# Kernel tuning notes

Measured on AMD Instinct MI355X. Metric: run time of the kernel, lower is better.

Reference implementation:

```python
import jax, jax.numpy as jnp
import numpy as np

FP8_MAX = 448.0   # float8_e4m3fn max magnitude
BS = 128          # quantization block size


def setup_inputs() -> dict:
    key = jax.random.key(0)
    k1, k2 = jax.random.split(key)
    M, K, N = 4096, 4096, 16384
    x = jax.random.normal(k1, (M, K), jnp.float32)
    # Build an FP8 block-quantized weight the way load() expects it:
    # weight holds fp8-representable values, weight_scale_inv is per 128x128 block.
    w = jax.random.normal(k2, (N, K), jnp.float32) * 0.02
    wb = w.reshape(N // BS, BS, K // BS, BS)
    amax = jnp.max(jnp.abs(wb), axis=(1, 3))            # [N/BS, K/BS]
    weight_scale_inv = amax / FP8_MAX                    # fp32 block scales
    wq = (wb / weight_scale_inv[:, None, :, None]).astype(jnp.float8_e4m3fn)
    weight = wq.astype(jnp.float32).reshape(N, K)        # fp8 values held in fp32
    return {"x": x, "weight": weight, "weight_scale_inv": weight_scale_inv}


def reference(x, weight, weight_scale_inv):
    M, K = x.shape
    N = weight.shape[0]
    # --- act_quant: per-(row, 128-block) FP8 quantization of activations ---
    xb = x.reshape(M, K // BS, BS)
    s_x = jnp.max(jnp.abs(xb), axis=-1) / FP8_MAX        # [M, K/BS] fp32 scales
    xq = (xb / s_x[..., None]).astype(jnp.float8_e4m3fn) # simulate fp8 rounding
    # --- fp8_gemm: scaled GEMM with inline dequantization ---
    x_dq = (xq.astype(jnp.float32) * s_x[..., None]).reshape(M, K)
    w_dq = (weight.reshape(N // BS, BS, K // BS, BS)
            * weight_scale_inv[:, None, :, None]).reshape(N, K)
    # y[m, n] = sum_k x_dq[m, k] * w_dq[n, k]
    return jnp.einsum('mk,nk->mn', x_dq, w_dq)
```

## Files before the change

### kernel.cpp

```cpp
#include <hip/hip_runtime.h>
#include <stdint.h>

#define FP8_MAX 448.0f
#define BSQ 128
#define TM 128
#define TN 128
#define NKB 32

typedef int   i32x4  __attribute__((ext_vector_type(4)));
typedef int   i32x8  __attribute__((ext_vector_type(8)));
typedef float f32x4v __attribute__((ext_vector_type(4)));
typedef float f32x16 __attribute__((ext_vector_type(16)));

typedef const __attribute__((address_space(1))) uint8_t* gptr_t;
typedef __attribute__((address_space(3))) uint8_t* lptr_t;

__device__ __forceinline__ int hsw(int row) { return (row ^ (row >> 3)) & 7; }

__global__ void act_quant_kernel(const float* __restrict__ x,
                                 uint8_t* __restrict__ xq,
                                 float* __restrict__ sxT,
                                 int M, int K) {
    int gid  = blockIdx.x * blockDim.x + threadIdx.x;
    int wave = gid >> 6;
    int lane = threadIdx.x & 63;
    int nkb  = K / BSQ;
    int row  = wave / nkb;
    int kb   = wave - row * nkb;
    if (row >= M) return;

    const float2 v = *(const float2*)(x + (size_t)row * K + kb * BSQ + lane * 2);
    float am = fmaxf(fabsf(v.x), fabsf(v.y));
#pragma unroll
    for (int off = 32; off >= 1; off >>= 1)
        am = fmaxf(am, __shfl_xor(am, off));

    float s = am / FP8_MAX;
    if (lane == 0) sxT[(size_t)kb * M + row] = s;

    float q0 = (am > 0.f) ? v.x / s : 0.f;
    float q1 = (am > 0.f) ? v.y / s : 0.f;
    int packed = __builtin_amdgcn_cvt_pk_fp8_f32(q0, q1, 0, false);
    *(uint16_t*)(xq + (size_t)row * K + kb * BSQ + lane * 2) = (uint16_t)(packed & 0xffff);
}

__global__ void weight_quant_kernel(const float* __restrict__ w,
                                    uint8_t* __restrict__ wq, size_t n) {
    size_t i = ((size_t)blockIdx.x * blockDim.x + threadIdx.x) * 4;
    if (i >= n) return;
    float4 v = *(const float4*)(w + i);
    int lo = __builtin_amdgcn_cvt_pk_fp8_f32(v.x, v.y, 0, false);
    int hi = __builtin_amdgcn_cvt_pk_fp8_f32(v.z, v.w, 0, false);
    *(uint32_t*)(wq + i) = (uint32_t)((lo & 0xffff) | (hi << 16));
}

__global__ __launch_bounds__(256, 2)
void fp8_gemm_mx(const uint8_t* __restrict__ Aq,
                 const uint8_t* __restrict__ Bq,
                 const float*  __restrict__ sxT,
                 const float*  __restrict__ swg,
                 float* __restrict__ out,
                 int M, int N, int K) {
    __shared__ uint8_t As[2][TM * BSQ];
    __shared__ uint8_t Bs[2][TN * BSQ];
    __shared__ float   sxs[2][TM];

    const int tid  = threadIdx.x;
    const int lane = tid & 63;
    const int wid  = tid >> 6;
    const int brow = blockIdx.y * TM;
    const int bcol = blockIdx.x * TN;
    const int nb   = bcol >> 7;

    const int wy = wid >> 1, wx = wid & 1;
    const int fl = lane & 31, hi = lane >> 5;

    auto STAGE = [&](int buf, int kb) {
#pragma unroll
        for (int r = 0; r < 4; ++r) {
            int slot = r * 256 + tid;
            int row  = slot >> 3;
            int g    = (slot & 7) ^ hsw(row);
            const uint8_t* gA = Aq + (size_t)(brow + row) * K + kb * BSQ + g * 16;
            const uint8_t* gB = Bq + (size_t)(bcol + row) * K + kb * BSQ + g * 16;
            __builtin_amdgcn_global_load_lds((gptr_t)gA,
                (lptr_t)(As[buf] + (slot & ~63) * 16), 16, 0, 0);
            __builtin_amdgcn_global_load_lds((gptr_t)gB,
                (lptr_t)(Bs[buf] + (slot & ~63) * 16), 16, 0, 0);
        }
        if (wid < 2) {
            const float* gs = sxT + (size_t)kb * M + brow + wid * 64 + lane;
            __builtin_amdgcn_global_load_lds((gptr_t)(const uint8_t*)gs,
                (lptr_t)(sxs[buf] + wid * 64), 4, 0, 0);
        }
    };

    const f32x16 zz = {0.f,0.f,0.f,0.f, 0.f,0.f,0.f,0.f,
                       0.f,0.f,0.f,0.f, 0.f,0.f,0.f,0.f};
    f32x16 acc[2][2];
#pragma unroll
    for (int i = 0; i < 2; ++i)
#pragma unroll
        for (int j = 0; j < 2; ++j) acc[i][j] = zz;

    STAGE(0, 0);
    __syncthreads();

    for (int kb = 0; kb < NKB; ++kb) {
        const int cur = kb & 1;
        const uint8_t* Ab = As[cur];
        const uint8_t* Bb = Bs[cur];
        const float*   Sb = sxs[cur];

        if (kb + 1 < NKB) STAGE(cur ^ 1, kb + 1);

        const float sw = swg[(size_t)nb * NKB + kb];

        i32x8 bfr[2][2];
#pragma unroll
        for (int fn = 0; fn < 2; ++fn) {
            int row = wx * 64 + fn * 32 + fl;
            int hh  = hsw(row);
            const uint8_t* base = Bb + row * BSQ;
#pragma unroll
            for (int kh = 0; kh < 2; ++kh) {
                int g0 = kh * 4 + hi * 2;
                i32x4 lo = *(const i32x4*)(base + (((g0    ) ^ hh) << 4));
                i32x4 h4 = *(const i32x4*)(base + (((g0 + 1) ^ hh) << 4));
                bfr[fn][kh] = (i32x8){lo.x, lo.y, lo.z, lo.w, h4.x, h4.y, h4.z, h4.w};
            }
        }

#pragma unroll
        for (int fm = 0; fm < 2; ++fm) {
            int arow = wy * 64 + fm * 32 + fl;
            int hh   = hsw(arow);
            const uint8_t* abase = Ab + arow * BSQ;
            i32x8 afr[2];
#pragma unroll
            for (int kh = 0; kh < 2; ++kh) {
                int g0 = kh * 4 + hi * 2;
                i32x4 lo = *(const i32x4*)(abase + (((g0    ) ^ hh) << 4));
                i32x4 h4 = *(const i32x4*)(abase + (((g0 + 1) ^ hh) << 4));
                afr[kh] = (i32x8){lo.x, lo.y, lo.z, lo.w, h4.x, h4.y, h4.z, h4.w};
            }
            f32x4v s4[4];
#pragma unroll
            for (int q = 0; q < 4; ++q) {
                s4[q] = *(const f32x4v*)&Sb[wy * 64 + fm * 32 + q * 8 + hi * 4];
                s4[q] *= sw;
            }

#pragma unroll
            for (int fn = 0; fn < 2; ++fn) {
                f32x16 p = __builtin_amdgcn_mfma_scale_f32_32x32x64_f8f6f4(
                    afr[0], bfr[fn][0], zz, 0, 0, 0, 127, 0, 127);
                p = __builtin_amdgcn_mfma_scale_f32_32x32x64_f8f6f4(
                    afr[1], bfr[fn][1], p, 0, 0, 0, 127, 0, 127);
#pragma unroll
                for (int q = 0; q < 4; ++q)
#pragma unroll
                    for (int j = 0; j < 4; ++j)
                        acc[fm][fn][q * 4 + j] += p[q * 4 + j] * s4[q][j];
            }
        }

        __syncthreads();
    }

#pragma unroll
    for (int fm = 0; fm < 2; ++fm)
#pragma unroll
        for (int fn = 0; fn < 2; ++fn)
#pragma unroll
            for (int q = 0; q < 4; ++q)
#pragma unroll
                for (int j = 0; j < 4; ++j) {
                    int row = brow + wy * 64 + fm * 32 + q * 8 + hi * 4 + j;
                    int col = bcol + wx * 64 + fn * 32 + fl;
                    __builtin_nontemporal_store(acc[fm][fn][q * 4 + j],
                                                &out[(size_t)row * N + col]);
                }
}

extern "C" void kernel_launch(void* const* d_in, const int* in_sizes, int n_in,
                              void* d_out, int out_size, void* d_ws, size_t ws_size,
                              hipStream_t stream) {
    const float* x   = (const float*)d_in[0];
    const float* w   = (const float*)d_in[1];
    const float* wsi = (const float*)d_in[2];
    float* out = (float*)d_out;

    const int K = 4096;
    const int M = in_sizes[0] / K;
    const int N = in_sizes[1] / K;

    uint8_t* xq  = (uint8_t*)d_ws;
    uint8_t* wq  = xq + (size_t)M * K;
    float*   sxT = (float*)(wq + (size_t)N * K);

    int waves = M * (K / BSQ);
    act_quant_kernel<<<dim3(waves / 4), dim3(256), 0, stream>>>(x, xq, sxT, M, K);

    size_t wn = (size_t)N * K;
    weight_quant_kernel<<<dim3((unsigned)(wn / 4 / 256)), dim3(256), 0, stream>>>(w, wq, wn);

    dim3 grid(N / TN, M / TM);
    fp8_gemm_mx<<<grid, dim3(256), 0, stream>>>(xq, wq, sxT, wsi, out, M, N, K);
}
```

Measured before the change: 458.4 us.

## Split K-block staging into two phases with fine-grained vmcnt waits and barriers

Replaces the single STAGE-plus-__syncthreads double buffering with a split prefetch. The B tile, scales and the first half of the A rows are issued after the B fragments are read, and the second half of the A rows after the first A fragment group is consumed. Explicit s_waitcnt vmcnt counts and raw s_barrier calls let each fm half start once only its own data has landed. It also interleaves the two MFMA chains and raises wave priority around them. The hand-counted vmcnt values depend on the exact number of global_load_lds instructions issued per lane, so a miscount could race or stall.

After: 478.1 us. 1.04x slower.

```diff
diff --git a/kernel.cpp b/kernel.cpp
--- a/kernel.cpp
+++ b/kernel.cpp
@@ -75,23 +75,48 @@
     const int wy = wid >> 1, wx = wid & 1;
     const int fl = lane & 31, hi = lane >> 5;
 
-    auto STAGE = [&](int buf, int kb) {
-#pragma unroll
-        for (int r = 0; r < 4; ++r) {
+    auto ISSUE7 = [&](int buf, int kb) {
+        {
+            if (lane < 32) {
+                const float* gs = sxT + (size_t)kb * M + brow + wid * 32 + lane;
+                __builtin_amdgcn_global_load_lds((gptr_t)(const uint8_t*)gs,
+                    (lptr_t)(sxs[buf] + wid * 32), 4, 0, 0);
+            }
+        }
+#pragma unroll
+        for (int h = 0; h < 2; ++h)
+#pragma unroll
+            for (int r = 0; r < 2; ++r) {
+                int slot = r * 256 + tid;
+                int row  = h * 64 + (slot >> 3);
+                int g    = (slot & 7) ^ hsw(row);
+                const uint8_t* gB = Bq + (size_t)(bcol + row) * K + kb * BSQ + g * 16;
+                __builtin_amdgcn_global_load_lds((gptr_t)gB,
+                    (lptr_t)(Bs[buf] + h * 8192 + (slot & ~63) * 16), 16, 0, 0);
+            }
+#pragma unroll
+        for (int r = 0; r < 2; ++r) {
             int slot = r * 256 + tid;
-            int row  = slot >> 3;
+            int rp   = slot >> 3;
+            int row  = (rp & 31) + ((rp & 32) << 1);
             int g    = (slot & 7) ^ hsw(row);
             const uint8_t* gA = Aq + (size_t)(brow + row) * K + kb * BSQ + g * 16;
-            const uint8_t* gB = Bq + (size_t)(bcol + row) * K + kb * BSQ + g * 16;
+            int rp0  = (r * 256 + wid * 64) >> 3;
             __builtin_amdgcn_global_load_lds((gptr_t)gA,
-                (lptr_t)(As[buf] + (slot & ~63) * 16), 16, 0, 0);
-            __builtin_amdgcn_global_load_lds((gptr_t)gB,
-                (lptr_t)(Bs[buf] + (slot & ~63) * 16), 16, 0, 0);
-        }
-        if (wid < 2) {
-            const float* gs = sxT + (size_t)kb * M + brow + wid * 64 + lane;
-            __builtin_amdgcn_global_load_lds((gptr_t)(const uint8_t*)gs,
-                (lptr_t)(sxs[buf] + wid * 64), 4, 0, 0);
+                (lptr_t)(As[buf] + ((rp0 & 31) + ((rp0 & 32) << 1)) * 128), 16, 0, 0);
+        }
+    };
+    auto ISSUE2 = [&](int buf, int kb) {
+#pragma unroll
+        for (int r = 0; r < 2; ++r) {
+            int slot = r * 256 + tid;
+            int rp   = slot >> 3;
+            int row  = 32 + (rp & 31) + ((rp & 32) << 1);
+            int g    = (slot & 7) ^ hsw(row);
+            const uint8_t* gA = Aq + (size_t)(brow + row) * K + kb * BSQ + g * 16;
+            int rp0  = (r * 256 + wid * 64) >> 3;
+            __builtin_amdgcn_global_load_lds((gptr_t)gA,
+                (lptr_t)(As[buf] + (32 + (rp0 & 31) + ((rp0 & 32) << 1)) * 128), 16, 0, 0);
         }
     };
 
@@ -103,18 +128,20 @@
 #pragma unroll
         for (int j = 0; j < 2; ++j) acc[i][j] = zz;
 
-    STAGE(0, 0);
-    __syncthreads();
+    ISSUE7(0, 0);
+    ISSUE2(0, 0);
 
     for (int kb = 0; kb < NKB; ++kb) {
         const int cur = kb & 1;
+        const bool pf = (kb + 1 < NKB);
         const uint8_t* Ab = As[cur];
         const uint8_t* Bb = Bs[cur];
         const float*   Sb = sxs[cur];
-
-        if (kb + 1 < NKB) STAGE(cur ^ 1, kb + 1);
-
         const float sw = swg[(size_t)nb * NKB + kb];
+
+        asm volatile("s_waitcnt vmcnt(2)" ::: "memory");
+        __builtin_amdgcn_s_barrier();
+        asm volatile("" ::: "memory");
 
         i32x8 bfr[2][2];
 #pragma unroll
@@ -131,8 +158,17 @@
             }
         }
 
+        if (pf) ISSUE7(cur ^ 1, kb + 1);
+
 #pragma unroll
         for (int fm = 0; fm < 2; ++fm) {
+            if (fm == 1) {
+                if (pf) asm volatile("s_waitcnt vmcnt(7)" ::: "memory");
+                else    asm volatile("s_waitcnt vmcnt(0)" ::: "memory");
+                __builtin_amdgcn_s_barrier();
+                asm volatile("" ::: "memory");
+            }
+
             int arow = wy * 64 + fm * 32 + fl;
             int hh   = hsw(arow);
             const uint8_t* abase = Ab + arow * BSQ;
@@ -151,21 +187,27 @@
                 s4[q] *= sw;
             }
 
-#pragma unroll
-            for (int fn = 0; fn < 2; ++fn) {
-                f32x16 p = __builtin_amdgcn_mfma_scale_f32_32x32x64_f8f6f4(
-                    afr[0], bfr[fn][0], zz, 0, 0, 0, 127, 0, 127);
-                p = __builtin_amdgcn_mfma_scale_f32_32x32x64_f8f6f4(
-                    afr[1], bfr[fn][1], p, 0, 0, 0, 127, 0, 127);
-#pragma unroll
-                for (int q = 0; q < 4; ++q)
-#pragma unroll
-                    for (int j = 0; j < 4; ++j)
-                        acc[fm][fn][q * 4 + j] += p[q * 4 + j] * s4[q][j];
-            }
-        }
-
-        __syncthreads();
+            if (fm == 1 && pf) ISSUE2(cur ^ 1, kb + 1);
+
+            __builtin_amdgcn_s_setprio(1);
+            f32x16 p0 = __builtin_amdgcn_mfma_scale_f32_32x32x64_f8f6f4(
+                afr[0], bfr[0][0], zz, 0, 0, 0, 127, 0, 127);
+            p0 = __builtin_amdgcn_mfma_scale_f32_32x32x64_f8f6f4(
+                afr[1], bfr[0][1], p0, 0, 0, 0, 127, 0, 127);
+            f32x16 p1 = __builtin_amdgcn_mfma_scale_f32_32x32x64_f8f6f4(
+                afr[0], bfr[1][0], zz, 0, 0, 0, 127, 0, 127);
+            p1 = __builtin_amdgcn_mfma_scale_f32_32x32x64_f8f6f4(
+                afr[1], bfr[1][1], p1, 0, 0, 0, 127, 0, 127);
+            __builtin_amdgcn_s_setprio(0);
+
+#pragma unroll
+            for (int q = 0; q < 4; ++q)
+#pragma unroll
+                for (int j = 0; j < 4; ++j) {
+                    acc[fm][0][q * 4 + j] += p0[q * 4 + j] * s4[q][j];
+                    acc[fm][1][q * 4 + j] += p1[q * 4 + j] * s4[q][j];
+                }
+        }
     }
 
 #pragma unroll
```
